# Kernel optimization log

Hardware: AMD Instinct MI355X
Metric: run time of the kernel (lower is better)

## Reference

```python
import jax, jax.numpy as jnp
import numpy as np

D_MODEL = 1024
N_HEADS = 16
HEAD_DIM = D_MODEL // N_HEADS
ROPE_BASE = 10000.0


def rope_rot(t, pos):
    # t: [B, L, H, hd], pos: [L] int32 absolute positions. Rotate-half RoPE.
    hd = t.shape[-1]
    inv_freq = 1.0 / (ROPE_BASE ** (jnp.arange(0, hd, 2, dtype=jnp.float32) / hd))
    freqs = pos.astype(jnp.float32)[:, None] * inv_freq[None, :]  # [L, hd/2]
    cos = jnp.cos(freqs)[None, :, None, :]  # [1, L, 1, hd/2]
    sin = jnp.sin(freqs)[None, :, None, :]
    t1, t2 = t[..., : hd // 2], t[..., hd // 2 :]
    return jnp.concatenate([t1 * cos - t2 * sin, t2 * cos + t1 * sin], axis=-1)


def setup_inputs() -> dict:
    key = jax.random.key(0)
    ks = jax.random.split(key, 8)
    B, L, S = 8, 16, 8192
    x = jax.random.normal(ks[0], (B, L, D_MODEL), dtype=jnp.float32)
    cache_k = jax.random.normal(ks[1], (B, S, N_HEADS, HEAD_DIM), dtype=jnp.float32)
    cache_v = jax.random.normal(ks[2], (B, S, N_HEADS, HEAD_DIM), dtype=jnp.float32)
    sc = 1.0 / np.sqrt(D_MODEL)
    qkv_w = jax.random.normal(ks[3], (D_MODEL, 3 * D_MODEL), dtype=jnp.float32) * sc
    qkv_b = jnp.zeros((3 * D_MODEL,), dtype=jnp.float32)
    o_w = jax.random.normal(ks[4], (D_MODEL, D_MODEL), dtype=jnp.float32) * sc
    o_b = jnp.zeros((D_MODEL,), dtype=jnp.float32)
    return {
        "x": x,
        "cache_k": cache_k,
        "cache_v": cache_v,
        "qkv_w": qkv_w,
        "qkv_b": qkv_b,
        "o_w": o_w,
        "o_b": o_b,
        "cache_index": S,
    }


def reference(x, cache_k, cache_v, qkv_w, qkv_b, o_w, o_b, cache_index):
    B, L, _ = x.shape
    qkv = x @ qkv_w + qkv_b  # [B, L, 3*d]
    q, k, v = jnp.split(qkv, 3, axis=-1)
    q = q.reshape(B, L, N_HEADS, HEAD_DIM)
    k = k.reshape(B, L, N_HEADS, HEAD_DIM)
    v = v.reshape(B, L, N_HEADS, HEAD_DIM)
    pos = cache_index + jnp.arange(L, dtype=jnp.int32)
    q = rope_rot(q, pos)
    k = rope_rot(k, pos)
    # streaming: append new k/v to cache (cached entries already RoPE-rotated)
    k_full = jnp.concatenate([cache_k, k], axis=1)  # [B, S+L, H, hd]
    v_full = jnp.concatenate([cache_v, v], axis=1)
    scale = 1.0 / jnp.sqrt(jnp.asarray(HEAD_DIM, dtype=q.dtype))
    scores = jnp.einsum("blhd,bshd->bhls", q, k_full) * scale  # [B, H, L, S+L]
    probs = jax.nn.softmax(scores, axis=-1)  # no mask in original module
    out = jnp.einsum("bhls,bshd->blhd", probs, v_full)
    out = out.reshape(B, L, D_MODEL)
    return out @ o_w + o_b
```

## Files before the change

### kernel.cpp

```cpp
#include <hip/hip_runtime.h>

#define B_ 8
#define L_ 16
#define H_ 16
#define D_ 64
#define DM 1024
#define S_ 8192

__device__ __forceinline__ void gld_lds16(const float* g, float* l) {
  __builtin_amdgcn_global_load_lds(
      (const __attribute__((address_space(1))) void*)g,
      (__attribute__((address_space(3))) void*)l, 16, 0, 0);
}

template <int CTRL>
__device__ __forceinline__ float add_dpp(float x) {
  int y = __builtin_amdgcn_update_dpp(0, __float_as_int(x), CTRL, 0xf, 0xf, false);
  return x + __int_as_float(y);
}

__global__ void __launch_bounds__(256) gemm_splitk_kernel(
    const float* __restrict__ A, const float* __restrict__ W,
    float* __restrict__ part, int lda, int ldw, int Kchunk)
{
  const int c0 = blockIdx.x * 64;
  const int k0 = blockIdx.y * Kchunk;
  const int t  = threadIdx.x;
  __shared__ float xs[32][132];
  __shared__ float wsm[32][64];
  float acc[8][4];
  #pragma unroll
  for (int i = 0; i < 8; ++i)
    #pragma unroll
    for (int j = 0; j < 4; ++j) acc[i][j] = 0.f;
  const int rg = t >> 4, cg = t & 15;
  const int r0 = rg * 8, ct0 = cg * 4;
  for (int ks = 0; ks < Kchunk; ks += 32) {
    __syncthreads();
    #pragma unroll
    for (int i = 0; i < 4; ++i) {
      int fi = t + i * 256;
      int r = fi >> 3, kq = fi & 7;
      float4 v = *(const float4*)(A + (size_t)r * lda + k0 + ks + kq * 4);
      xs[kq*4+0][r] = v.x; xs[kq*4+1][r] = v.y;
      xs[kq*4+2][r] = v.z; xs[kq*4+3][r] = v.w;
    }
    #pragma unroll
    for (int i = 0; i < 2; ++i) {
      int si = t + i * 256;
      int kk = si >> 4, cq = si & 15;
      *(float4*)&wsm[kk][cq*4] =
          *(const float4*)(W + (size_t)(k0 + ks + kk) * ldw + c0 + cq * 4);
    }
    __syncthreads();
    #pragma unroll
    for (int kk = 0; kk < 32; ++kk) {
      float a[8], bb[4];
      *(float4*)&a[0] = *(const float4*)&xs[kk][r0];
      *(float4*)&a[4] = *(const float4*)&xs[kk][r0 + 4];
      *(float4*)&bb[0] = *(const float4*)&wsm[kk][ct0];
      #pragma unroll
      for (int ii = 0; ii < 8; ++ii)
        #pragma unroll
        for (int jj = 0; jj < 4; ++jj)
          acc[ii][jj] = fmaf(a[ii], bb[jj], acc[ii][jj]);
    }
  }
  float* po = part + (size_t)blockIdx.y * 128 * ldw;
  #pragma unroll
  for (int ii = 0; ii < 8; ++ii)
    #pragma unroll
    for (int jj = 0; jj < 4; ++jj)
      po[(size_t)(r0 + ii) * ldw + c0 + ct0 + jj] = acc[ii][jj];
}

__global__ void ropefuse_kernel(const float* __restrict__ part,
                                const float* __restrict__ bias,
                                const int* __restrict__ cidx,
                                float* __restrict__ qh, float* __restrict__ kn,
                                float* __restrict__ vn)
{
  int gt = blockIdx.x * 256 + threadIdx.x;
  int i = gt & 31, l = (gt >> 5) & 15, h = (gt >> 9) & 15, b = gt >> 13;
  int row = b * L_ + l;
  const int PS = 128 * 3072;
  const float* pr = part + (size_t)row * 3072;
  int cq = h * 64 + i;
  int cols[6] = {cq, cq + 32, 1024 + cq, 1024 + cq + 32, 2048 + cq, 2048 + cq + 32};
  float v[6];
  #pragma unroll
  for (int c = 0; c < 6; ++c) {
    float s = bias[cols[c]];
    #pragma unroll
    for (int ks = 0; ks < 4; ++ks) s += pr[(size_t)ks * PS + cols[c]];
    v[c] = s;
  }
  int pos = cidx[0] + l;
  float inv = exp2f((float)i * (-13.287712379549449f / 32.0f));
  float fr = (float)pos * inv;
  float sn, cs;
  sincosf(fr, &sn, &cs);
  int ob = ((b * H_ + h) * L_ + l) * 64;
  qh[ob + i]      = (v[0] * cs - v[1] * sn) * 0.125f;
  qh[ob + 32 + i] = (v[1] * cs + v[0] * sn) * 0.125f;
  kn[ob + i]      = v[2] * cs - v[3] * sn;
  kn[ob + 32 + i] = v[3] * cs + v[2] * sn;
  vn[ob + i]      = v[4];
  vn[ob + 32 + i] = v[5];
}

__global__ void __launch_bounds__(512, 4) attn_partial_kernel(
    const float* __restrict__ qh, const float* __restrict__ kc,
    const float* __restrict__ vc, float* __restrict__ opart,
    float* __restrict__ lpart)
{
  const int chunk = blockIdx.x;
  const int b     = blockIdx.y;
  const int tid   = threadIdx.x;
  const int w = tid >> 6, lane = tid & 63;
  const int h = tid >> 5, dq = (tid >> 2) & 7, lg = tid & 3;
  __shared__ float kv[4 * 4096];

  float4 q0[4], q1[4], o0[4], o1[4];
  {
    const float* qb = qh + ((size_t)b * 256 + h * 16 + lg * 4) * 64 + dq * 8;
    #pragma unroll
    for (int li = 0; li < 4; ++li) {
      q0[li] = *(const float4*)(qb + li * 64);
      q1[li] = *(const float4*)(qb + li * 64 + 4);
      o0[li].x = o0[li].y = o0[li].z = o0[li].w = 0.f;
      o1[li].x = o1[li].y = o1[li].z = o1[li].w = 0.f;
    }
  }
  float l_run[4] = {0.f, 0.f, 0.f, 0.f};

  const size_t kbase = (size_t)b * S_ * DM;
  const int st0 = chunk * 128;
  const int rS = (w >> 1) & 1, sub = w & 1;
  const float* stream = (w < 4) ? kc : vc;
  const int srcoff = 8 * lane + 4 * sub;

  auto issue = [&](int T) {
    const float* rowp = stream + kbase + (size_t)(st0 + T * 2 + rS) * DM + srcoff;
    float* dst = &kv[(T & 3) * 4096 + w * 512];
    gld_lds16(rowp, dst);
    gld_lds16(rowp + 512, dst + 256);
  };

  issue(0); issue(1); issue(2);

  const int g4 = 4 * (h * 8 + dq);

#define STEP(T, WAITOP) do {                                                  \
    asm volatile(WAITOP ::: "memory");                                        \
    __builtin_amdgcn_sched_barrier(0);                                        \
    __builtin_amdgcn_s_barrier();                                             \
    if ((T) + 3 < 64) issue((T) + 3);                                         \
    const float* u = &kv[((T) & 3) * 4096];                                   \
    _Pragma("unroll")                                                         \
    for (int r = 0; r < 2; ++r) {                                             \
      const float* kp = u + r * 1024 + g4;                                    \
      float4 ka  = *(const float4*)kp;                                        \
      float4 kb2 = *(const float4*)(kp + 512);                                \
      float4 va  = *(const float4*)(kp + 2048);                               \
      float4 vb2 = *(const float4*)(kp + 2560);                               \
      float pex[4];                                                           \
      _Pragma("unroll")                                                       \
      for (int li = 0; li < 4; ++li) {                                        \
        float sc = ka.x*q0[li].x + ka.y*q0[li].y + ka.z*q0[li].z + ka.w*q0[li].w \
                 + kb2.x*q1[li].x + kb2.y*q1[li].y + kb2.z*q1[li].z + kb2.w*q1[li].w; \
        sc = add_dpp<0x124>(sc);           \
        sc = add_dpp<0x128>(sc);           \
        sc += __shfl_xor(sc, 16);        \
        pex[li] = __expf(sc);                                                 \
        l_run[li] += pex[li];                                                 \
      }                                                                       \
      _Pragma("unroll")                                                       \
      for (int li = 0; li < 4; ++li) {                                        \
        o0[li].x = fmaf(pex[li], va.x,  o0[li].x);                            \
        o0[li].y = fmaf(pex[li], va.y,  o0[li].y);                            \
        o0[li].z = fmaf(pex[li], va.z,  o0[li].z);                            \
        o0[li].w = fmaf(pex[li], va.w,  o0[li].w);                            \
        o1[li].x = fmaf(pex[li], vb2.x, o1[li].x);                            \
        o1[li].y = fmaf(pex[li], vb2.y, o1[li].y);                            \
        o1[li].z = fmaf(pex[li], vb2.z, o1[li].z);                            \
        o1[li].w = fmaf(pex[li], vb2.w, o1[li].w);                            \
      }                                                                       \
    } } while (0)

  for (int t = 0; t < 62; ++t) STEP(t, "s_waitcnt vmcnt(4)");
  STEP(62, "s_waitcnt vmcnt(2)");
  STEP(63, "s_waitcnt vmcnt(0)");
#undef STEP

  const size_t ob = (((size_t)(b * 64 + chunk) * 16 + h) * 16 + lg * 4) * 64 + dq * 8;
  #pragma unroll
  for (int li = 0; li < 4; ++li) {
    *(float4*)&opart[ob + (size_t)li * 64]     = o0[li];
    *(float4*)&opart[ob + (size_t)li * 64 + 4] = o1[li];
  }
  if (dq == 0) {
    #pragma unroll
    for (int li = 0; li < 4; ++li)
      lpart[((b * 64 + chunk) * 16 + h) * 16 + lg * 4 + li] = l_run[li];
  }
}

__global__ void __launch_bounds__(64) combine_kernel(
    const float* __restrict__ qh, const float* __restrict__ kn,
    const float* __restrict__ vn, const float* __restrict__ opart,
    const float* __restrict__ lpart, float* __restrict__ attn)
{
  const int bh = blockIdx.x;
  const int b = bh >> 4, h = bh & 15;
  const int l0 = blockIdx.y * 4;
  const int lane = threadIdx.x;
  __shared__ float kb[1024], vb[1024], qb[256];
  __shared__ float scn[4][16];
  for (int i = 0; i < 16; ++i) {
    kb[i * 64 + lane] = kn[(size_t)(bh * 16 + i) * 64 + lane];
    vb[i * 64 + lane] = vn[(size_t)(bh * 16 + i) * 64 + lane];
  }
  {
    int ll = lane >> 4, sl = lane & 15;
    *(float4*)&qb[ll * 64 + sl * 4] =
        *(const float4*)&qh[(size_t)(bh * 16 + l0 + ll) * 64 + sl * 4];
  }
  __syncthreads();
  {
    int ll = lane >> 4, sp = lane & 15;
    float a = 0.f;
    for (int d = 0; d < 64; ++d) a += qb[ll * 64 + d] * kb[sp * 64 + d];
    scn[ll][sp] = a;
  }
  __syncthreads();
  for (int ll = 0; ll < 4; ++ll) {
    const int l = l0 + ll;
    float den = 0.f, od = 0.f;
    for (int c = 0; c < 64; ++c) {
      den += lpart[((b * 64 + c) * 16 + h) * 16 + l];
      od  += opart[(((size_t)(b * 64 + c) * 16 + h) * 16 + l) * 64 + lane];
    }
    #pragma unroll
    for (int sp = 0; sp < 16; ++sp) {
      float pex = __expf(scn[ll][sp]);
      den += pex;
      od += pex * vb[sp * 64 + lane];
    }
    attn[((size_t)(b * 16 + l) * 16 + h) * 64 + lane] = od / den;
  }
}

__global__ void reduce_out_kernel(const float* __restrict__ part2,
                                  const float* __restrict__ ob,
                                  float* __restrict__ out)
{
  int idx = blockIdx.x * 256 + threadIdx.x;
  int c = idx & 1023;
  float s = ob[c];
  #pragma unroll
  for (int ks = 0; ks < 8; ++ks) s += part2[(size_t)ks * 131072 + idx];
  out[idx] = s;
}

extern "C" void kernel_launch(void* const* d_in, const int* in_sizes, int n_in,
                              void* d_out, int out_size, void* d_ws, size_t ws_size,
                              hipStream_t stream) {
  (void)in_sizes; (void)n_in; (void)out_size; (void)ws_size;
  const float* x       = (const float*)d_in[0];
  const float* cache_k = (const float*)d_in[1];
  const float* cache_v = (const float*)d_in[2];
  const float* qkv_w   = (const float*)d_in[3];
  const float* qkv_b   = (const float*)d_in[4];
  const float* o_w     = (const float*)d_in[5];
  const float* o_b     = (const float*)d_in[6];
  const int*   cidx    = (const int*)d_in[7];
  float* out = (float*)d_out;

  float* ws    = (float*)d_ws;
  float* big   = ws;
  float* part1 = big;
  float* opart = big;
  float* part2 = big;
  float* qh    = big + 8388608;
  float* kn    = qh + 131072;
  float* vn    = kn + 131072;
  float* lpart = vn + 131072;
  float* attn  = lpart + 131072;

  gemm_splitk_kernel<<<dim3(48, 4), 256, 0, stream>>>(x, qkv_w, part1, 1024, 3072, 256);
  ropefuse_kernel<<<256, 256, 0, stream>>>(part1, qkv_b, cidx, qh, kn, vn);
  attn_partial_kernel<<<dim3(64, 8), 512, 0, stream>>>(qh, cache_k, cache_v,
                                                       opart, lpart);
  combine_kernel<<<dim3(128, 4), 64, 0, stream>>>(qh, kn, vn, opart, lpart, attn);
  gemm_splitk_kernel<<<dim3(16, 8), 256, 0, stream>>>(attn, o_w, part2, 1024, 1024, 128);
  reduce_out_kernel<<<512, 256, 0, stream>>>(part2, o_b, out);
}
```

Before: 224.0 us.

## Replace LDS-staged KV pipeline with direct register double-buffered global loads

The attention partial kernel no longer stages K/V rows through shared memory with async global-to-LDS loads and block barriers. Each thread now loads its own K and V slices straight from global memory into registers, double-buffered one row ahead. This removes the LDS traffic and the per-step workgroup barriers. In exchange it gives up deeper prefetch, so the loop may stall on memory latency and need more registers. The last iteration loads row 127 a second time instead of branching.

Result: slower. 311.8 us (+39.2%).

```diff
diff --git a/kernel.cpp b/kernel.cpp
--- a/kernel.cpp
+++ b/kernel.cpp
@@ -6,12 +6,6 @@
 #define D_ 64
 #define DM 1024
 #define S_ 8192
-
-__device__ __forceinline__ void gld_lds16(const float* g, float* l) {
-  __builtin_amdgcn_global_load_lds(
-      (const __attribute__((address_space(1))) void*)g,
-      (__attribute__((address_space(3))) void*)l, 16, 0, 0);
-}
 
 template <int CTRL>
 __device__ __forceinline__ float add_dpp(float x) {
@@ -117,9 +111,7 @@
   const int chunk = blockIdx.x;
   const int b     = blockIdx.y;
   const int tid   = threadIdx.x;
-  const int w = tid >> 6, lane = tid & 63;
   const int h = tid >> 5, dq = (tid >> 2) & 7, lg = tid & 3;
-  __shared__ float kv[4 * 4096];
 
   float4 q0[4], q1[4], o0[4], o1[4];
   {
@@ -134,64 +126,54 @@
   }
   float l_run[4] = {0.f, 0.f, 0.f, 0.f};
 
-  const size_t kbase = (size_t)b * S_ * DM;
-  const int st0 = chunk * 128;
-  const int rS = (w >> 1) & 1, sub = w & 1;
-  const float* stream = (w < 4) ? kc : vc;
-  const int srcoff = 8 * lane + 4 * sub;
-
-  auto issue = [&](int T) {
-    const float* rowp = stream + kbase + (size_t)(st0 + T * 2 + rS) * DM + srcoff;
-    float* dst = &kv[(T & 3) * 4096 + w * 512];
-    gld_lds16(rowp, dst);
-    gld_lds16(rowp + 512, dst + 256);
+  const size_t rbase = (size_t)b * S_ * DM + (size_t)chunk * 128 * DM + h * 64 + dq * 8;
+  const float* kp = kc + rbase;
+  const float* vp = vc + rbase;
+
+  float4 kA0, kA1, vA0, vA1, kB0, kB1, vB0, vB1;
+
+#define LOADR(K0, K1, V0, V1, R) do {                                         \
+    const float* kq_ = kp + (size_t)(R) * DM;                                 \
+    const float* vq_ = vp + (size_t)(R) * DM;                                 \
+    K0 = *(const float4*)kq_;  K1 = *(const float4*)(kq_ + 4);                \
+    V0 = *(const float4*)vq_;  V1 = *(const float4*)(vq_ + 4);                \
+  } while (0)
+
+  auto compute = [&](const float4& K0, const float4& K1,
+                     const float4& V0, const float4& V1) {
+    float pex[4];
+    #pragma unroll
+    for (int li = 0; li < 4; ++li) {
+      float sc = K0.x*q0[li].x + K0.y*q0[li].y + K0.z*q0[li].z + K0.w*q0[li].w
+               + K1.x*q1[li].x + K1.y*q1[li].y + K1.z*q1[li].z + K1.w*q1[li].w;
+      sc = add_dpp<0x124>(sc);
+      sc = add_dpp<0x128>(sc);
+      sc += __shfl_xor(sc, 16);
+      pex[li] = __expf(sc);
+      l_run[li] += pex[li];
+    }
+    #pragma unroll
+    for (int li = 0; li < 4; ++li) {
+      o0[li].x = fmaf(pex[li], V0.x, o0[li].x);
+      o0[li].y = fmaf(pex[li], V0.y, o0[li].y);
+      o0[li].z = fmaf(pex[li], V0.z, o0[li].z);
+      o0[li].w = fmaf(pex[li], V0.w, o0[li].w);
+      o1[li].x = fmaf(pex[li], V1.x, o1[li].x);
+      o1[li].y = fmaf(pex[li], V1.y, o1[li].y);
+      o1[li].z = fmaf(pex[li], V1.z, o1[li].z);
+      o1[li].w = fmaf(pex[li], V1.w, o1[li].w);
+    }
   };
 
-  issue(0); issue(1); issue(2);
-
-  const int g4 = 4 * (h * 8 + dq);
-
-#define STEP(T, WAITOP) do {                                                  \
-    asm volatile(WAITOP ::: "memory");                                        \
-    __builtin_amdgcn_sched_barrier(0);                                        \
-    __builtin_amdgcn_s_barrier();                                             \
-    if ((T) + 3 < 64) issue((T) + 3);                                         \
-    const float* u = &kv[((T) & 3) * 4096];                                   \
-    _Pragma("unroll")                                                         \
-    for (int r = 0; r < 2; ++r) {                                             \
-      const float* kp = u + r * 1024 + g4;                                    \
-      float4 ka  = *(const float4*)kp;                                        \
-      float4 kb2 = *(const float4*)(kp + 512);                                \
-      float4 va  = *(const float4*)(kp + 2048);                               \
-      float4 vb2 = *(const float4*)(kp + 2560);                               \
-      float pex[4];                                                           \
-      _Pragma("unroll")                                                       \
-      for (int li = 0; li < 4; ++li) {                                        \
-        float sc = ka.x*q0[li].x + ka.y*q0[li].y + ka.z*q0[li].z + ka.w*q0[li].w \
-                 + kb2.x*q1[li].x + kb2.y*q1[li].y + kb2.z*q1[li].z + kb2.w*q1[li].w; \
-        sc = add_dpp<0x124>(sc);           \
-        sc = add_dpp<0x128>(sc);           \
-        sc += __shfl_xor(sc, 16);        \
-        pex[li] = __expf(sc);                                                 \
-        l_run[li] += pex[li];                                                 \
-      }                                                                       \
-      _Pragma("unroll")                                                       \
-      for (int li = 0; li < 4; ++li) {                                        \
-        o0[li].x = fmaf(pex[li], va.x,  o0[li].x);                            \
-        o0[li].y = fmaf(pex[li], va.y,  o0[li].y);                            \
-        o0[li].z = fmaf(pex[li], va.z,  o0[li].z);                            \
-        o0[li].w = fmaf(pex[li], va.w,  o0[li].w);                            \
-        o1[li].x = fmaf(pex[li], vb2.x, o1[li].x);                            \
-        o1[li].y = fmaf(pex[li], vb2.y, o1[li].y);                            \
-        o1[li].z = fmaf(pex[li], vb2.z, o1[li].z);                            \
-        o1[li].w = fmaf(pex[li], vb2.w, o1[li].w);                            \
-      }                                                                       \
-    } } while (0)
-
-  for (int t = 0; t < 62; ++t) STEP(t, "s_waitcnt vmcnt(4)");
-  STEP(62, "s_waitcnt vmcnt(2)");
-  STEP(63, "s_waitcnt vmcnt(0)");
-#undef STEP
+  LOADR(kA0, kA1, vA0, vA1, 0);
+  for (int t = 0; t < 128; t += 2) {
+    LOADR(kB0, kB1, vB0, vB1, t + 1);
+    compute(kA0, kA1, vA0, vA1);
+    const int rn = (t + 2 < 128) ? (t + 2) : 127;
+    LOADR(kA0, kA1, vA0, vA1, rn);
+    compute(kB0, kB1, vB0, vB1);
+  }
+#undef LOADR
 
   const size_t ob = (((size_t)(b * 64 + chunk) * 16 + h) * 16 + lg * 4) * 64 + dq * 8;
   #pragma unroll
```
